# Performance work log

Measured on AMD Instinct MI355X. Metric: run time of the kernel, lower is better.

## Reference

```python
import jax, jax.numpy as jnp
import numpy as np

IN_DIM, H_DIM, OUT_DIM, N_LAYERS = 128, 512, 128, 3
B, S = 32, 1024


def setup_inputs() -> dict:
    key = jax.random.key(0)
    ks = jax.random.split(key, 20)
    def lin(k, out_d, in_d, scale=None):
        s = scale if scale is not None else 1.0 / np.sqrt(in_d)
        return jax.random.uniform(k, (out_d, in_d), jnp.float32, -s, s)
    def bias(k, out_d, in_d):
        s = 1.0 / np.sqrt(in_d)
        return jax.random.uniform(k, (out_d,), jnp.float32, -s, s)
    inp = {
        "x": jax.random.normal(ks[0], (B, S, IN_DIM), jnp.float32),
        "h0": jax.random.normal(ks[1], (B, N_LAYERS, H_DIM), jnp.float32),
        # layer-0 input->hidden gates (with bias)
        "W0z": lin(ks[2], H_DIM, IN_DIM), "b0z": bias(ks[3], H_DIM, IN_DIM),
        "W0r": lin(ks[4], H_DIM, IN_DIM), "b0r": bias(ks[5], H_DIM, IN_DIM),
        "W0g": lin(ks[6], H_DIM, IN_DIM), "b0g": bias(ks[7], H_DIM, IN_DIM),
        # shared input->hidden gates for layers >= 1 (with bias)
        "Wxz": lin(ks[8], H_DIM, H_DIM), "bxz": bias(ks[9], H_DIM, H_DIM),
        "Wxr": lin(ks[10], H_DIM, H_DIM), "bxr": bias(ks[11], H_DIM, H_DIM),
        "Wxg": lin(ks[12], H_DIM, H_DIM), "bxg": bias(ks[13], H_DIM, H_DIM),
        # shared hidden->hidden gates for ALL layers (no bias)
        "Whz": lin(ks[14], H_DIM, H_DIM),
        "Whr": lin(ks[15], H_DIM, H_DIM),
        "Whg": lin(ks[16], H_DIM, H_DIM),
        # output projection
        "Wout": lin(ks[17], OUT_DIM, H_DIM), "bout": bias(ks[18], OUT_DIM, H_DIM),
    }
    return inp


def _gru_forward(x, h0, W0z, b0z, W0r, b0r, W0g, b0g,
                 Wxz, bxz, Wxr, bxr, Wxg, bxg, Whz, Whr, Whg, Wout, bout):
    # Precompute layer-0 input projections for all timesteps: (S, B, H)
    xz0 = jnp.einsum('bsi,hi->sbh', x, W0z) + b0z
    xr0 = jnp.einsum('bsi,hi->sbh', x, W0r) + b0r
    xg0 = jnp.einsum('bsi,hi->sbh', x, W0g) + b0g

    hs0 = jnp.swapaxes(h0, 0, 1)  # (L, B, H)

    def cell(xz, xr, xg, h):
        z = jax.nn.sigmoid(xz + h @ Whz.T)
        r = jax.nn.sigmoid(xr + h @ Whr.T)
        g = jnp.tanh(xg + (r * h) @ Whg.T)
        return z * h + (1.0 - z) * g

    def step(hs, inp_t):
        xz, xr, xg = inp_t
        new_hs = []
        h = cell(xz, xr, xg, hs[0])
        new_hs.append(h)
        inp = h
        for j in range(1, N_LAYERS):
            h = cell(inp @ Wxz.T + bxz, inp @ Wxr.T + bxr, inp @ Wxg.T + bxg, hs[j])
            new_hs.append(h)
            inp = h
        out_t = inp @ Wout.T + bout  # (B, O)
        return jnp.stack(new_hs), out_t

    hs_final, outs = jax.lax.scan(step, hs0, (xz0, xr0, xg0))
    layer_output = jnp.swapaxes(outs, 0, 1)       # (B, S, O)
    hidden_state = jnp.swapaxes(hs_final, 0, 1)   # (B, L, H)
    return layer_output, hidden_state


def reference(x, h0, W0z, b0z, W0r, b0r, W0g, b0g,
              Wxz, bxz, Wxr, bxr, Wxg, bxg, Whz, Whr, Whg, Wout, bout):
    return _gru_forward(x, h0, W0z, b0z, W0r, b0r, W0g, b0g,
                        Wxz, bxz, Wxr, bxr, Wxg, bxg, Whz, Whr, Whg, Wout, bout)
```

## Files before the change

### kernel.cpp

```cpp
#include <hip/hip_runtime.h>
#include <cstdint>
#include <cstddef>

#define B_   32
#define S_   1024
#define IN_  128
#define H_   512
#define OUT_ 128
#define NL_  3

typedef __attribute__((ext_vector_type(8))) short short8;
typedef __attribute__((ext_vector_type(4))) float floatx4;
typedef __attribute__((ext_vector_type(2))) unsigned uint2v;

constexpr size_t OFF_CLAIM = 0;
constexpr size_t OFF_P1L   = 128;
constexpr size_t OFF_P2L   = 512;
constexpr size_t OFF_P1R   = 896;
constexpr size_t OFF_P2R   = 1280;
constexpr size_t OFF_PO    = 1664;
constexpr size_t OFF_W0Z  = 8192;
constexpr size_t OFF_W0R  = OFF_W0Z + 131072;
constexpr size_t OFF_W0G  = OFF_W0R + 131072;
constexpr size_t OFF_WXZ  = OFF_W0G + 131072;
constexpr size_t OFF_WXR  = OFF_WXZ + 524288;
constexpr size_t OFF_WXG  = OFF_WXR + 524288;
constexpr size_t OFF_WHZ  = OFF_WXG + 524288;
constexpr size_t OFF_WHR  = OFF_WHZ + 524288;
constexpr size_t OFF_WHG  = OFF_WHR + 524288;
constexpr size_t OFF_WOUT = OFF_WHG + 524288;
constexpr size_t OFF_XBF  = OFF_WOUT + 131072;
constexpr size_t OFF_HST  = OFF_XBF + 8388608;
constexpr size_t OFF_HLOC = OFF_HST + 196608;
constexpr size_t OFF_HREM = OFF_HLOC + 393216;
constexpr size_t OFF_RH   = OFF_HREM + 393216;

__device__ __forceinline__ unsigned short f2bf(float f) {
    unsigned u = __float_as_uint(f);
    unsigned r = (u + 0x7FFFu + ((u >> 16) & 1u)) >> 16;
    return (unsigned short)r;
}
__device__ __forceinline__ float sigmoidf_(float x) { return 1.0f / (1.0f + __expf(-x)); }

__device__ __forceinline__ short8 load16_coh(const void* p) {
    union { unsigned long long u[2]; short8 s; } r;
    const unsigned long long* q = (const unsigned long long*)p;
    r.u[0] = __hip_atomic_load(q,     __ATOMIC_RELAXED, __HIP_MEMORY_SCOPE_AGENT);
    r.u[1] = __hip_atomic_load(q + 1, __ATOMIC_RELAXED, __HIP_MEMORY_SCOPE_AGENT);
    return r.s;
}
__device__ __forceinline__ void store8_coh(void* p, unsigned lo, unsigned hi) {
    uint2v u; u.x = lo; u.y = hi;
    asm volatile("global_store_dwordx2 %0, %1, off sc0 sc1" :: "v"(p), "v"(u) : "memory");
}

#define VDRAIN() asm volatile("s_waitcnt vmcnt(0)" ::: "memory")

__device__ __forceinline__ unsigned wave_min32_bcast(unsigned f) {
#pragma unroll
    for (int off = 1; off < 32; off <<= 1) {
        unsigned o = (unsigned)__shfl_xor((int)f, off, 64);
        f = (o < f) ? o : f;
    }
    return (unsigned)__shfl((int)f, 0, 64);
}
__device__ __forceinline__ unsigned poll_loc32(const unsigned* flags, unsigned thr, int skip, int lane) {
    const unsigned* p = flags + (lane & 31);
    unsigned f;
    for (;;) {
        f = __builtin_nontemporal_load(p);
        if ((lane & 31) == skip) f = 0xFFFFFFFFu;
        if (__all((int)(f >= thr))) break;
        asm volatile("s_sleep 1" ::: "memory");
    }
    return wave_min32_bcast(f);
}
__device__ __forceinline__ unsigned poll_rem32(const unsigned* flags, unsigned thr, int lane) {
    const unsigned* p = flags + (lane & 31);
    unsigned f;
    for (;;) {
        f = __hip_atomic_load(p, __ATOMIC_RELAXED, __HIP_MEMORY_SCOPE_AGENT);
        if (__all((int)(f >= thr))) break;
        asm volatile("s_sleep 2" ::: "memory");
    }
    return wave_min32_bcast(f);
}
__device__ __forceinline__ void st_flag_loc(unsigned* p, unsigned v) { __builtin_nontemporal_store(v, p); }
__device__ __forceinline__ void st_flag_rem(unsigned* p, unsigned v) {
    __hip_atomic_store(p, v, __ATOMIC_RELAXED, __HIP_MEMORY_SCOPE_AGENT);
}

__global__ void __launch_bounds__(1024) prep_kernel(
    const float* __restrict__ x, const float* __restrict__ h0,
    const float* __restrict__ W0z, const float* __restrict__ W0r, const float* __restrict__ W0g,
    const float* __restrict__ Wxz, const float* __restrict__ Wxr, const float* __restrict__ Wxg,
    const float* __restrict__ Whz, const float* __restrict__ Whr, const float* __restrict__ Whg,
    const float* __restrict__ Wout, char* __restrict__ ws)
{
    int i = blockIdx.x * 1024 + threadIdx.x;
    unsigned short* xbf = (unsigned short*)(ws + OFF_XBF);
    if (i < B_ * S_ * IN_) xbf[i] = f2bf(x[i]);
    if (i < 65536) {
        ((unsigned short*)(ws + OFF_W0Z))[i]  = f2bf(W0z[i]);
        ((unsigned short*)(ws + OFF_W0R))[i]  = f2bf(W0r[i]);
        ((unsigned short*)(ws + OFF_W0G))[i]  = f2bf(W0g[i]);
        ((unsigned short*)(ws + OFF_WOUT))[i] = f2bf(Wout[i]);
    }
    if (i < 262144) {
        ((unsigned short*)(ws + OFF_WXZ))[i] = f2bf(Wxz[i]);
        ((unsigned short*)(ws + OFF_WXR))[i] = f2bf(Wxr[i]);
        ((unsigned short*)(ws + OFF_WXG))[i] = f2bf(Wxg[i]);
        ((unsigned short*)(ws + OFF_WHZ))[i] = f2bf(Whz[i]);
        ((unsigned short*)(ws + OFF_WHR))[i] = f2bf(Whr[i]);
        ((unsigned short*)(ws + OFF_WHG))[i] = f2bf(Whg[i]);
    }
    if (i < B_ * NL_ * H_) {
        int b = i / (NL_ * H_); int r = i % (NL_ * H_); int j = r / H_; int n = r % H_;
        float v = h0[i];
        ((float*)(ws + OFF_HST))[(j * B_ + b) * H_ + n] = v;
        ((unsigned short*)(ws + OFF_HLOC))[((j * 4 + 3) * B_ + b) * H_ + n] = f2bf(v);
    }
    if (i < 448) {
        unsigned v = 0u;
        int rel = i - (int)(OFF_PO / 4);
        if (rel >= 8 && rel < 32) v = 0xFFFFFFFFu;
        ((unsigned*)ws)[i] = v;
    }
}

__global__ void __launch_bounds__(256, 1) gru_kernel(char* ws,
    const float* __restrict__ b0z, const float* __restrict__ b0r, const float* __restrict__ b0g,
    const float* __restrict__ bxz, const float* __restrict__ bxr, const float* __restrict__ bxg,
    const float* __restrict__ bout, float* __restrict__ out)
{
    __shared__ int role_s;
    if (threadIdx.x == 0) {
        int xcc;
        asm volatile("s_getreg_b32 %0, hwreg(HW_REG_XCC_ID, 0, 32)" : "=s"(xcc));
        xcc &= 7;
        int role = -1;
        unsigned slot = atomicAdd((unsigned*)(ws + OFF_CLAIM) + xcc, 1u);
        if (xcc < 3)       { if (slot < 32) role = xcc * 32 + (int)slot; }
        else if (xcc == 3) { if (slot < 8)  role = 96 + (int)slot; }
        role_s = role;
    }
    __syncthreads();
    const int role = role_s;
    if (role < 0) return;

    const bool is_out = (role >= 96);
    const int tid   = threadIdx.x;
    const int v     = tid >> 6;
    const int lane  = tid & 63;
    const int btile = v & 1;
    const int khalf = v >> 1;
    const int l15   = lane & 15;
    const int quad  = lane >> 4;
    const int koff  = quad * 8;
    const int arow  = btile * 16 + l15;

    __shared__ float part[4][2][256];
    __shared__ short8 wrl[2][16][64];

    const int j  = is_out ? 0 : (role >> 5);
    const int nt = role & 31;
    const int nrow = nt * 16 + l15;
    const int Tx = (j == 0) ? 4 : 16;
    const int T1 = Tx + 16;
    short8 wzc[16], wgc[16];
    const short* xbf = (const short*)(ws + OFF_XBF);
    float* hst = (float*)(ws + OFF_HST) + (size_t)j * B_ * H_;
    unsigned short* hloc = (unsigned short*)(ws + OFF_HLOC);
    unsigned short* hrem = (unsigned short*)(ws + OFF_HREM);
    unsigned short* rh_j = (unsigned short*)(ws + OFF_RH) + (size_t)j * B_ * H_;

    unsigned* p1l = (unsigned*)(ws + OFF_P1L) + j * 32;
    unsigned* p2l = (unsigned*)(ws + OFF_P2L) + j * 32;
    unsigned* p1r_self = (unsigned*)(ws + OFF_P1R) + j * 32;
    unsigned* p2r_self = (unsigned*)(ws + OFF_P2R) + j * 32;
    unsigned* p2r_low  = (unsigned*)(ws + OFF_P2R) + (j - 1) * 32;
    unsigned* warfl    = (j < 2) ? (unsigned*)(ws + OFF_P1R) + (j + 1) * 32
                                 : (unsigned*)(ws + OFF_PO);
    unsigned* p2r2 = (unsigned*)(ws + OFF_P2R) + 2 * 32;
    unsigned* pofl = (unsigned*)(ws + OFF_PO);

    const int ont = role - 96;
    short8 wc[8];

    const int rb  = tid >> 2;
    const int bq  = rb >> 4;
    const int bl  = rb & 15;
    const int rnl = (tid & 3) * 4;
    float4 brv4 = {0,0,0,0}, bzv4 = {0,0,0,0}, bgv4 = {0,0,0,0}, bov4 = {0,0,0,0};

    if (!is_out) {
        const float* bz_b = (j == 0) ? b0z : bxz;
        const float* br_b = (j == 0) ? b0r : bxr;
        const float* bg_b = (j == 0) ? b0g : bxg;
        if (tid < 128) {
            bzv4 = *(const float4*)(bz_b + nt * 16 + rnl);
            brv4 = *(const float4*)(br_b + nt * 16 + rnl);
            bgv4 = *(const float4*)(bg_b + nt * 16 + rnl);
        }
        const int strx = (j == 0) ? IN_ : H_;
        const short* Wz_x = (const short*)(ws + ((j == 0) ? OFF_W0Z : OFF_WXZ));
        const short* Wr_x = (const short*)(ws + ((j == 0) ? OFF_W0R : OFF_WXR));
        const short* Wg_x = (const short*)(ws + ((j == 0) ? OFF_W0G : OFF_WXG));
        const short* Wz_h = (const short*)(ws + OFF_WHZ);
        const short* Wr_h = (const short*)(ws + OFF_WHR);
        const short* Wg_h = (const short*)(ws + OFF_WHG);
#pragma unroll
        for (int kt = 0; kt < 16; ++kt) {
            int g = khalf * 16 + kt;
            if (g < T1) {
                if (g < Tx) {
                    long o = (long)nrow * strx + g * 32 + koff;
                    wzc[kt] = *(const short8*)(Wz_x + o);
                    wgc[kt] = *(const short8*)(Wg_x + o);
                    wrl[khalf][kt][lane] = *(const short8*)(Wr_x + o);
                } else {
                    long o = (long)nrow * H_ + (g - Tx) * 32 + koff;
                    wzc[kt] = *(const short8*)(Wz_h + o);
                    wgc[kt] = *(const short8*)(Wg_h + o);
                    wrl[khalf][kt][lane] = *(const short8*)(Wr_h + o);
                }
            }
        }
    } else {
        const short* Wo = (const short*)(ws + OFF_WOUT);
        if (tid < 128) bov4 = *(const float4*)(bout + ont * 16 + rnl);
#pragma unroll
        for (int kt = 0; kt < 8; ++kt) {
            int g = khalf * 8 + kt;
            wc[kt] = *(const short8*)(Wo + (long)(ont * 16 + l15) * H_ + g * 32 + koff);
        }
    }
    __syncthreads();

    if (!is_out) {
        short8 afrag[16];
        float zacc[4], hv[4];
        unsigned defer_lo = 0, defer_hi = 0;
        unsigned memoA = 0, memoB = 0, memoC = 0, memoD = 0;

#pragma unroll 1
        for (int t = 0; t < S_; ++t) {
            if (memoA < (unsigned)t) memoA = poll_loc32(p2l, t, nt, lane);
            if (j > 0 && memoB < (unsigned)(t + 1)) memoB = poll_rem32(p2r_low, t + 1, lane);

            if (t > 0 && tid < 128)
                store8_coh(hrem + ((size_t)(j * 4 + ((t - 1) & 3)) * B_ + rb) * H_ + nt * 16 + rnl,
                           defer_lo, defer_hi);

            {
                const unsigned short* hl = hloc + (size_t)(j * 4 + ((t - 1) & 3)) * B_ * H_;
                const unsigned short* ir = (j > 0) ? hrem + (size_t)((j - 1) * 4 + (t & 3)) * B_ * H_ : nullptr;
#pragma unroll
                for (int kt = 0; kt < 16; ++kt) {
                    int g = khalf * 16 + kt;
                    if (g < T1) {
                        if (g < Tx) {
                            if (j == 0) afrag[kt] = *(const short8*)(xbf + (long)arow * (S_ * IN_) + (long)t * IN_ + g * 32 + koff);
                            else        afrag[kt] = load16_coh(ir + (long)arow * H_ + g * 32 + koff);
                        } else {
                            afrag[kt] = __builtin_nontemporal_load(
                                (const short8*)(hl + (long)arow * H_ + (g - Tx) * 32 + koff));
                        }
                    }
                }
            }
            {
                floatx4 az = {0.f, 0.f, 0.f, 0.f}, ar = {0.f, 0.f, 0.f, 0.f};
#pragma unroll
                for (int kt = 0; kt < 16; ++kt) {
                    int g = khalf * 16 + kt;
                    if (g < T1) {
                        short8 wr = wrl[khalf][kt][lane];
                        az = __builtin_amdgcn_mfma_f32_16x16x32_bf16(afrag[kt], wzc[kt], az, 0, 0, 0);
                        ar = __builtin_amdgcn_mfma_f32_16x16x32_bf16(afrag[kt], wr, ar, 0, 0, 0);
                    }
                }
#pragma unroll
                for (int i = 0; i < 4; ++i) {
                    int e = (quad * 4 + i) * 16 + l15;
                    part[v][0][e] = az[i];
                    part[v][1][e] = ar[i];
                }
            }
            __syncthreads();
            if (tid < 128) {
                float4 h4 = *(const float4*)(hst + rb * H_ + nt * 16 + rnl);
                unsigned lo = 0, hi = 0;
#pragma unroll
                for (int m = 0; m < 4; ++m) {
                    int e = bl * 16 + rnl + m;
                    float zs = part[bq][0][e] + part[bq + 2][0][e];
                    float rs = part[bq][1][e] + part[bq + 2][1][e];
                    zacc[m] = zs;
                    hv[m] = h4[m];
                    float r = sigmoidf_(rs + brv4[m]);
                    unsigned p = (unsigned)f2bf(r * h4[m]) << (16 * (m & 1));
                    if (m < 2) lo |= p; else hi |= p;
                }
                unsigned long long pk = (unsigned long long)lo | ((unsigned long long)hi << 32);
                __builtin_nontemporal_store(pk, (unsigned long long*)(rh_j + rb * H_ + nt * 16 + rnl));
            }
            VDRAIN();
            __syncthreads();
            if (tid == 0) {
                st_flag_loc(&p1l[nt], t + 1);
                if (j > 0) st_flag_rem(&p1r_self[nt], t + 1);
                if (t > 0) st_flag_rem(&p2r_self[nt], t);
            }

            if (memoC < (unsigned)(t + 1)) memoC = poll_loc32(p1l, t + 1, nt, lane);
            if (t >= 4) {
                unsigned thr = (unsigned)(t - 3);
                if (memoD < thr) memoD = poll_rem32(warfl, thr, lane);
            }
#pragma unroll
            for (int kt = 0; kt < 16; ++kt) {
                int g = khalf * 16 + kt;
                if (g >= Tx && g < T1)
                    afrag[kt] = __builtin_nontemporal_load(
                        (const short8*)((const unsigned short*)rh_j + (long)arow * H_ + (g - Tx) * 32 + koff));
            }
            {
                floatx4 ag = {0.f, 0.f, 0.f, 0.f};
#pragma unroll
                for (int kt = 0; kt < 16; ++kt) {
                    int g = khalf * 16 + kt;
                    if (g < T1)
                        ag = __builtin_amdgcn_mfma_f32_16x16x32_bf16(afrag[kt], wgc[kt], ag, 0, 0, 0);
                }
#pragma unroll
                for (int i = 0; i < 4; ++i) {
                    int e = (quad * 4 + i) * 16 + l15;
                    part[v][0][e] = ag[i];
                }
            }
            __syncthreads();
            if (tid < 128) {
                float4 h4n;
                unsigned lo = 0, hi = 0;
#pragma unroll
                for (int m = 0; m < 4; ++m) {
                    int e = bl * 16 + rnl + m;
                    float gs = part[bq][0][e] + part[bq + 2][0][e];
                    float gv = tanhf(gs + bgv4[m]);
                    float z  = sigmoidf_(zacc[m] + bzv4[m]);
                    float hn = z * hv[m] + (1.0f - z) * gv;
                    h4n[m] = hn;
                    unsigned p = (unsigned)f2bf(hn) << (16 * (m & 1));
                    if (m < 2) lo |= p; else hi |= p;
                }
                *(float4*)(hst + rb * H_ + nt * 16 + rnl) = h4n;
                unsigned long long pk = (unsigned long long)lo | ((unsigned long long)hi << 32);
                __builtin_nontemporal_store(pk,
                    (unsigned long long*)(hloc + ((size_t)(j * 4 + (t & 3)) * B_ + rb) * H_ + nt * 16 + rnl));
                defer_lo = lo; defer_hi = hi;
            }
            VDRAIN();
            __syncthreads();
            if (tid == 0) st_flag_loc(&p2l[nt], t + 1);
        }
        if (tid < 128)
            store8_coh(hrem + ((size_t)(j * 4 + 3) * B_ + rb) * H_ + nt * 16 + rnl, defer_lo, defer_hi);
        VDRAIN();
        __syncthreads();
        if (tid == 0) st_flag_rem(&p2r_self[nt], S_);
    } else {
        unsigned memoE = 0;
#pragma unroll 1
        for (int t = 0; t < S_; ++t) {
            if (memoE < (unsigned)(t + 1)) memoE = poll_rem32(p2r2, t + 1, lane);
            const unsigned short* h2 = hrem + (size_t)(2 * 4 + (t & 3)) * B_ * H_;
            short8 aoc[8];
#pragma unroll
            for (int kt = 0; kt < 8; ++kt) {
                int g = khalf * 8 + kt;
                aoc[kt] = load16_coh(h2 + (long)arow * H_ + g * 32 + koff);
            }
            floatx4 ao = {0.f, 0.f, 0.f, 0.f};
#pragma unroll
            for (int kt = 0; kt < 8; ++kt)
                ao = __builtin_amdgcn_mfma_f32_16x16x32_bf16(aoc[kt], wc[kt], ao, 0, 0, 0);
#pragma unroll
            for (int i = 0; i < 4; ++i) {
                int e = (quad * 4 + i) * 16 + l15;
                part[v][0][e] = ao[i];
            }
            __syncthreads();
            if (tid < 128) {
                float4 o4;
#pragma unroll
                for (int m = 0; m < 4; ++m) {
                    int e = bl * 16 + rnl + m;
                    o4[m] = part[bq][0][e] + part[bq + 2][0][e] + bov4[m];
                }
                *(float4*)(out + (long)rb * (S_ * OUT_) + (long)t * OUT_ + ont * 16 + rnl) = o4;
            }
            VDRAIN();
            __syncthreads();
            if (tid == 0) st_flag_rem(&pofl[ont], t + 1);
        }
    }
}

__global__ void __launch_bounds__(256) tail_kernel(const char* __restrict__ ws, float* __restrict__ out)
{
    int i = blockIdx.x * 256 + threadIdx.x;
    if (i < B_ * NL_ * H_) {
        int b = i / (NL_ * H_); int r = i % (NL_ * H_); int j = r / H_; int n = r % H_;
        out[B_ * S_ * OUT_ + i] = ((const float*)(ws + OFF_HST))[(j * B_ + b) * H_ + n];
    }
}

extern "C" void kernel_launch(void* const* d_in, const int* in_sizes, int n_in,
                              void* d_out, int out_size, void* d_ws, size_t ws_size,
                              hipStream_t stream)
{
    const float* x   = (const float*)d_in[0];
    const float* h0  = (const float*)d_in[1];
    const float* W0z = (const float*)d_in[2];  const float* b0z = (const float*)d_in[3];
    const float* W0r = (const float*)d_in[4];  const float* b0r = (const float*)d_in[5];
    const float* W0g = (const float*)d_in[6];  const float* b0g = (const float*)d_in[7];
    const float* Wxz = (const float*)d_in[8];  const float* bxz = (const float*)d_in[9];
    const float* Wxr = (const float*)d_in[10]; const float* bxr = (const float*)d_in[11];
    const float* Wxg = (const float*)d_in[12]; const float* bxg = (const float*)d_in[13];
    const float* Whz = (const float*)d_in[14];
    const float* Whr = (const float*)d_in[15];
    const float* Whg = (const float*)d_in[16];
    const float* Wout = (const float*)d_in[17]; const float* bout = (const float*)d_in[18];
    char* ws = (char*)d_ws;
    float* out = (float*)d_out;

    prep_kernel<<<dim3(4096), dim3(1024), 0, stream>>>(
        x, h0, W0z, W0r, W0g, Wxz, Wxr, Wxg, Whz, Whr, Whg, Wout, ws);

    gru_kernel<<<dim3(512), dim3(256), 0, stream>>>(
        ws, b0z, b0r, b0g, bxz, bxr, bxg, bout, out);

    tail_kernel<<<dim3(192), dim3(256), 0, stream>>>((const char*)ws, out);
}
```

Baseline: 8.144 ms.

## Split gate matmuls to overlap input projection with hidden-state polling; publish remote state immediately

```diff
diff --git a/kernel.cpp b/kernel.cpp
--- a/kernel.cpp
+++ b/kernel.cpp
@@ -41,6 +41,10 @@
     return (unsigned short)r;
 }
 __device__ __forceinline__ float sigmoidf_(float x) { return 1.0f / (1.0f + __expf(-x)); }
+__device__ __forceinline__ float tanhf_(float x) {
+    float e = __expf(2.0f * x);
+    return 1.0f - 2.0f / (e + 1.0f);
+}
 
 __device__ __forceinline__ short8 load16_coh(const void* p) {
     union { unsigned long long u[2]; short8 s; } r;
@@ -240,52 +244,57 @@
     if (!is_out) {
         short8 afrag[16];
         float zacc[4], hv[4];
-        unsigned defer_lo = 0, defer_hi = 0;
         unsigned memoA = 0, memoB = 0, memoC = 0, memoD = 0;
 
 #pragma unroll 1
         for (int t = 0; t < S_; ++t) {
+            if (j > 0 && memoB < (unsigned)(t + 1)) memoB = poll_rem32(p2r_low, t + 1, lane);
+            {
+                const unsigned short* ir = (j > 0) ? hrem + (size_t)((j - 1) * 4 + (t & 3)) * B_ * H_ : nullptr;
+#pragma unroll
+                for (int kt = 0; kt < 16; ++kt) {
+                    int g = khalf * 16 + kt;
+                    if (g < Tx) {
+                        if (j == 0) afrag[kt] = *(const short8*)(xbf + (long)arow * (S_ * IN_) + (long)t * IN_ + g * 32 + koff);
+                        else        afrag[kt] = load16_coh(ir + (long)arow * H_ + g * 32 + koff);
+                    }
+                }
+            }
+            floatx4 az = {0.f, 0.f, 0.f, 0.f}, ar = {0.f, 0.f, 0.f, 0.f};
+#pragma unroll
+            for (int kt = 0; kt < 16; ++kt) {
+                int g = khalf * 16 + kt;
+                if (g < Tx) {
+                    short8 wr = wrl[khalf][kt][lane];
+                    az = __builtin_amdgcn_mfma_f32_16x16x32_bf16(afrag[kt], wzc[kt], az, 0, 0, 0);
+                    ar = __builtin_amdgcn_mfma_f32_16x16x32_bf16(afrag[kt], wr, ar, 0, 0, 0);
+                }
+            }
             if (memoA < (unsigned)t) memoA = poll_loc32(p2l, t, nt, lane);
-            if (j > 0 && memoB < (unsigned)(t + 1)) memoB = poll_rem32(p2r_low, t + 1, lane);
-
-            if (t > 0 && tid < 128)
-                store8_coh(hrem + ((size_t)(j * 4 + ((t - 1) & 3)) * B_ + rb) * H_ + nt * 16 + rnl,
-                           defer_lo, defer_hi);
-
             {
                 const unsigned short* hl = hloc + (size_t)(j * 4 + ((t - 1) & 3)) * B_ * H_;
-                const unsigned short* ir = (j > 0) ? hrem + (size_t)((j - 1) * 4 + (t & 3)) * B_ * H_ : nullptr;
 #pragma unroll
                 for (int kt = 0; kt < 16; ++kt) {
                     int g = khalf * 16 + kt;
-                    if (g < T1) {
-                        if (g < Tx) {
-                            if (j == 0) afrag[kt] = *(const short8*)(xbf + (long)arow * (S_ * IN_) + (long)t * IN_ + g * 32 + koff);
-                            else        afrag[kt] = load16_coh(ir + (long)arow * H_ + g * 32 + koff);
-                        } else {
-                            afrag[kt] = __builtin_nontemporal_load(
-                                (const short8*)(hl + (long)arow * H_ + (g - Tx) * 32 + koff));
-                        }
-                    }
-                }
-            }
-            {
-                floatx4 az = {0.f, 0.f, 0.f, 0.f}, ar = {0.f, 0.f, 0.f, 0.f};
-#pragma unroll
-                for (int kt = 0; kt < 16; ++kt) {
-                    int g = khalf * 16 + kt;
-                    if (g < T1) {
-                        short8 wr = wrl[khalf][kt][lane];
-                        az = __builtin_amdgcn_mfma_f32_16x16x32_bf16(afrag[kt], wzc[kt], az, 0, 0, 0);
-                        ar = __builtin_amdgcn_mfma_f32_16x16x32_bf16(afrag[kt], wr, ar, 0, 0, 0);
-                    }
-                }
-#pragma unroll
-                for (int i = 0; i < 4; ++i) {
-                    int e = (quad * 4 + i) * 16 + l15;
-                    part[v][0][e] = az[i];
-                    part[v][1][e] = ar[i];
-                }
+                    if (g >= Tx && g < T1)
+                        afrag[kt] = __builtin_nontemporal_load(
+                            (const short8*)(hl + (long)arow * H_ + (g - Tx) * 32 + koff));
+                }
+            }
+#pragma unroll
+            for (int kt = 0; kt < 16; ++kt) {
+                int g = khalf * 16 + kt;
+                if (g >= Tx && g < T1) {
+                    short8 wr = wrl[khalf][kt][lane];
+                    az = __builtin_amdgcn_mfma_f32_16x16x32_bf16(afrag[kt], wzc[kt], az, 0, 0, 0);
+                    ar = __builtin_amdgcn_mfma_f32_16x16x32_bf16(afrag[kt], wr, ar, 0, 0, 0);
+                }
+            }
+#pragma unroll
+            for (int i = 0; i < 4; ++i) {
+                int e = (quad * 4 + i) * 16 + l15;
+                part[v][0][e] = az[i];
+                part[v][1][e] = ar[i];
             }
             __syncthreads();
             if (tid < 128) {
@@ -310,14 +319,17 @@
             if (tid == 0) {
                 st_flag_loc(&p1l[nt], t + 1);
                 if (j > 0) st_flag_rem(&p1r_self[nt], t + 1);
-                if (t > 0) st_flag_rem(&p2r_self[nt], t);
-            }
-
+            }
+
+            if (t >= 4 && memoD < (unsigned)(t - 3)) memoD = poll_rem32(warfl, t - 3, lane);
+            floatx4 ag = {0.f, 0.f, 0.f, 0.f};
+#pragma unroll
+            for (int kt = 0; kt < 16; ++kt) {
+                int g = khalf * 16 + kt;
+                if (g < Tx)
+                    ag = __builtin_amdgcn_mfma_f32_16x16x32_bf16(afrag[kt], wgc[kt], ag, 0, 0, 0);
+            }
             if (memoC < (unsigned)(t + 1)) memoC = poll_loc32(p1l, t + 1, nt, lane);
-            if (t >= 4) {
-                unsigned thr = (unsigned)(t - 3);
-                if (memoD < thr) memoD = poll_rem32(warfl, thr, lane);
-            }
 #pragma unroll
             for (int kt = 0; kt < 16; ++kt) {
                 int g = khalf * 16 + kt;
@@ -325,19 +337,16 @@
                     afrag[kt] = __builtin_nontemporal_load(
                         (const short8*)((const unsigned short*)rh_j + (long)arow * H_ + (g - Tx) * 32 + koff));
             }
-            {
-                floatx4 ag = {0.f, 0.f, 0.f, 0.f};
-#pragma unroll
-                for (int kt = 0; kt < 16; ++kt) {
-                    int g = khalf * 16 + kt;
-                    if (g < T1)
-                        ag = __builtin_amdgcn_mfma_f32_16x16x32_bf16(afrag[kt], wgc[kt], ag, 0, 0, 0);
-                }
-#pragma unroll
-                for (int i = 0; i < 4; ++i) {
-                    int e = (quad * 4 + i) * 16 + l15;
-                    part[v][0][e] = ag[i];
-                }
+#pragma unroll
+            for (int kt = 0; kt < 16; ++kt) {
+                int g = khalf * 16 + kt;
+                if (g >= Tx && g < T1)
+                    ag = __builtin_amdgcn_mfma_f32_16x16x32_bf16(afrag[kt], wgc[kt], ag, 0, 0, 0);
+            }
+#pragma unroll
+            for (int i = 0; i < 4; ++i) {
+                int e = (quad * 4 + i) * 16 + l15;
+                part[v][0][e] = ag[i];
             }
             __syncthreads();
             if (tid < 128) {
@@ -347,7 +356,7 @@
                 for (int m = 0; m < 4; ++m) {
                     int e = bl * 16 + rnl + m;
                     float gs = part[bq][0][e] + part[bq + 2][0][e];
-                    float gv = tanhf(gs + bgv4[m]);
+                    float gv = tanhf_(gs + bgv4[m]);
                     float z  = sigmoidf_(zacc[m] + bzv4[m]);
                     float hn = z * hv[m] + (1.0f - z) * gv;
                     h4n[m] = hn;
@@ -358,17 +367,15 @@
                 unsigned long long pk = (unsigned long long)lo | ((unsigned long long)hi << 32);
                 __builtin_nontemporal_store(pk,
                     (unsigned long long*)(hloc + ((size_t)(j * 4 + (t & 3)) * B_ + rb) * H_ + nt * 16 + rnl));
-                defer_lo = lo; defer_hi = hi;
+                store8_coh(hrem + ((size_t)(j * 4 + (t & 3)) * B_ + rb) * H_ + nt * 16 + rnl, lo, hi);
             }
             VDRAIN();
             __syncthreads();
-            if (tid == 0) st_flag_loc(&p2l[nt], t + 1);
+            if (tid == 0) {
+                st_flag_loc(&p2l[nt], t + 1);
+                st_flag_rem(&p2r_self[nt], t + 1);
+            }
         }
-        if (tid < 128)
-            store8_coh(hrem + ((size_t)(j * 4 + 3) * B_ + rb) * H_ + nt * 16 + rnl, defer_lo, defer_hi);
-        VDRAIN();
-        __syncthreads();
-        if (tid == 0) st_flag_rem(&p2r_self[nt], S_);
     } else {
         unsigned memoE = 0;
 #pragma unroll 1
```

Result: faster. 7.582 ms (-6.9%).
